# Kernel tuning notes

Measured on AMD Instinct MI355X. Metric: run time of the kernel, lower is better.

Reference implementation:

```python
import jax, jax.numpy as jnp
import numpy as np

B, T, C = 16, 1024, 1024
H = 4          # wshare
K = 31         # kernel_size


def setup_inputs() -> dict:
    key = jax.random.key(0)
    ks = jax.random.split(key, 8)
    s = 1.0 / np.sqrt(C)
    return {
        "query": jax.random.normal(ks[0], (B, T, C), jnp.float32),
        "key_t": jax.random.normal(ks[1], (B, T, C), jnp.float32),   # unused, API compat
        "value": jax.random.normal(ks[2], (B, T, C), jnp.float32),   # unused, API compat
        "mask": jnp.ones((B, 1, T), jnp.int32),
        "W1": jax.random.uniform(ks[3], (2 * C, C), jnp.float32, -s, s),
        "b1": jnp.zeros((2 * C,), jnp.float32),
        "W2": jax.random.uniform(ks[4], (C, C), jnp.float32, -s, s),
        "b2": jnp.zeros((C,), jnp.float32),
        "conv_w": jax.random.uniform(ks[5], (H, K), jnp.float32, 0.0, 1.0),
        "bias": jnp.zeros((C,), jnp.float32),
    }


def reference(query, key_t, value, mask, W1, b1, W2, b2, conv_w, bias):
    # linear1 + GLU: (B,T,C) -> (B,T,2C) -> (B,T,C)
    x = query @ W1.T + b1
    a, g = jnp.split(x, 2, axis=-1)
    x = a * jax.nn.sigmoid(g)
    # (B,T,C) -> (B,C,T) -> (B*C/H, H, T); channel c uses shared kernel c % H
    x = jnp.transpose(x, (0, 2, 1)).reshape(B * C // H, H, T)
    # softmax-normalized shared kernels (H,K); dropout_rate=0 (eval)
    w = jax.nn.softmax(conv_w, axis=-1)
    y = jax.lax.conv_general_dilated(
        x, w[:, None, :], window_strides=(1,), padding=[(K // 2, K // 2)],
        feature_group_count=H, dimension_numbers=("NCH", "OIH", "NCH"))
    x = y.reshape(B, C, T) + bias[None, :, None]
    x = jnp.transpose(x, (0, 2, 1))               # (B,T,C)
    # padding mask: (B,1,T) -> transpose(-1,-2) -> (B,T,1), zero masked frames
    m = jnp.transpose(mask, (0, 2, 1))
    x = jnp.where(m == 0, 0.0, x)
    return x @ W2.T + b2
```

## Files before the change

kernel.cpp:

```cpp
#include <hip/hip_runtime.h>

typedef __attribute__((ext_vector_type(8))) __bf16 bf16x8;
typedef __attribute__((ext_vector_type(4))) __bf16 bf16x4;
typedef __attribute__((ext_vector_type(4))) float  f32x4;
typedef __attribute__((ext_vector_type(4))) float  float4v;

#define DEV static __device__ __forceinline__

DEV void gload_lds16(const void* g, void* l) {
  __builtin_amdgcn_global_load_lds(
      (const __attribute__((address_space(1))) void*)g,
      (__attribute__((address_space(3))) void*)l, 16, 0, 0);
}

__global__ void cvt_bf16_kernel(const float* __restrict__ in,
                                __bf16* __restrict__ out, int n4) {
  int stride = gridDim.x * blockDim.x;
  for (int i = blockIdx.x * blockDim.x + threadIdx.x; i < n4; i += stride) {
    float4v v = ((const float4v*)in)[i];
    bf16x4 o;
#pragma unroll
    for (int j = 0; j < 4; ++j) o[j] = (__bf16)v[j];
    ((bf16x4*)out)[i] = o;
  }
}

__global__ void softmax_w_kernel(const float* __restrict__ cw,
                                 float* __restrict__ out) {
  int h = threadIdx.x;
  if (h < 4) {
    float m = cw[h * 31];
#pragma unroll
    for (int k = 1; k < 31; ++k) m = fmaxf(m, cw[h * 31 + k]);
    float e[31];
    float s = 0.f;
#pragma unroll
    for (int k = 0; k < 31; ++k) {
      e[k] = __expf(cw[h * 31 + k] - m);
      s += e[k];
    }
    float inv = 1.f / s;
#pragma unroll
    for (int k = 0; k < 31; ++k) out[h * 31 + k] = e[k] * inv;
  }
}

template <int STORE_BF16>
__global__ __launch_bounds__(512, 2)
void gemm256_kernel(const __bf16* __restrict__ A, const __bf16* __restrict__ Bw,
                    const float* __restrict__ bias, void* __restrict__ Cout,
                    int M, int N, int K, int ntn) {
  __shared__ __align__(16) __bf16 Al[4 * 8192];
  __shared__ __align__(16) __bf16 Bl[4 * 8192];

  const int tid  = threadIdx.x;
  const int lane = tid & 63;
  const int w    = tid >> 6;
  const int wm = w >> 2, wn = w & 3;

  const int nwg = gridDim.x;
  const int cpx = nwg >> 3;
  const int bid = blockIdx.x;
  const int wgid = (bid & 7) * cpx + (bid >> 3);
  const int m0 = (wgid / ntn) * 256;
  const int n0 = (wgid % ntn) * 256;

  const int NT = K >> 6;

  const int scolE = ((((tid & 7) * 16) ^ (((tid >> 3) & 7) << 4)) >> 1);
  const __bf16* __restrict__ Abase = A + (long)m0 * K;
  const __bf16* __restrict__ Bbase = Bw + (long)n0 * K;

  const int l15 = lane & 15;
  const int xk  = (l15 & 7) << 4;
  const int a0  = l15 * 128 + (((lane >> 4) * 16) ^ xk);
  const int a1  = l15 * 128 + ((((lane >> 4) * 16) + 64) ^ xk);
  const int bq  = (wn & 1) * 8192;
  const int b0  = bq + a0;
  const int b1  = bq + a1;

  f32x4 acc[8][4];
#pragma unroll
  for (int i = 0; i < 8; ++i)
#pragma unroll
    for (int j = 0; j < 4; ++j) {
      acc[i][j][0] = 0.f; acc[i][j][1] = 0.f;
      acc[i][j][2] = 0.f; acc[i][j][3] = 0.f;
    }
  bf16x8 af[8], bf[8];

#define ADST(p, mh) (Al + ((p) * 2 + (mh)) * 8192)
#define BDST(p, nh) (Bl + ((p) * 2 + (nh)) * 8192)
#define AWG(p) ((const char*)Al + ((p) * 2 + wm) * 16384)
#define BWG(p) ((const char*)Bl + ((p) * 2 + (wn >> 1)) * 16384)

#define STAGEG(base, groff, ktc, dst)                                         \
  {                                                                           \
    const __bf16* _s = (base) + (long)((groff) + (tid >> 3)) * K + (ktc) + scolE; \
    gload_lds16(_s, (dst) + tid * 8);                                         \
    gload_lds16(_s + (long)64 * K, (dst) + 4096 + tid * 8);                   \
  }

#define PH_MID()                                     \
  __builtin_amdgcn_s_barrier();                      \
  asm volatile("s_waitcnt lgkmcnt(0)" ::: "memory"); \
  __builtin_amdgcn_s_setprio(1);

#define PH_END(VM)                                                    \
  __builtin_amdgcn_s_setprio(0);                                      \
  if ((VM) == 4) asm volatile("s_waitcnt vmcnt(4)" ::: "memory");     \
  if ((VM) == 0) asm volatile("s_waitcnt vmcnt(0)" ::: "memory");     \
  __builtin_amdgcn_s_barrier();

#define RDA(IB, G)                                                \
  _Pragma("unroll") for (int i2 = 0; i2 < 4; ++i2) {              \
    af[i2 * 2 + 0] = *(const bf16x8*)((G) + ((IB) + i2) * 2048 + a0); \
    af[i2 * 2 + 1] = *(const bf16x8*)((G) + ((IB) + i2) * 2048 + a1); \
  }
#define RDB(JB, G)                                                \
  _Pragma("unroll") for (int j2 = 0; j2 < 2; ++j2) {              \
    bf[(JB) * 2 + j2 * 2 + 0] = *(const bf16x8*)((G) + ((JB) + j2) * 2048 + b0); \
    bf[(JB) * 2 + j2 * 2 + 1] = *(const bf16x8*)((G) + ((JB) + j2) * 2048 + b1); \
  }

#define MMQ(IB, JB)                                                           \
  _Pragma("unroll") for (int i2 = 0; i2 < 4; ++i2)                            \
  _Pragma("unroll") for (int j2 = 0; j2 < 2; ++j2)                            \
  _Pragma("unroll") for (int kk = 0; kk < 2; ++kk)                            \
      acc[(IB) + i2][(JB) + j2] = __builtin_amdgcn_mfma_f32_16x16x32_bf16(    \
          af[i2 * 2 + kk], bf[(JB) * 2 + j2 * 2 + kk], acc[(IB) + i2][(JB) + j2], 0, 0, 0);

  STAGEG(Abase, 0,   0, ADST(0, 0));
  STAGEG(Abase, 128, 0, ADST(0, 1));
  STAGEG(Bbase, 0,   0, BDST(0, 0));
  STAGEG(Bbase, 128, 0, BDST(0, 1));
  asm volatile("s_waitcnt vmcnt(0)" ::: "memory");
  __builtin_amdgcn_s_barrier();

#define TILE(tt, CUR)                                        \
  {                                                          \
    const int ktn = (((tt) + 1 < NT) ? (tt) + 1 : NT - 1) * 64; \
                                                    \
    RDA(0, AWG(CUR)); RDB(0, BWG(CUR));                      \
    STAGEG(Abase, 0,   ktn, ADST(CUR ^ 1, 0));               \
    STAGEG(Abase, 128, ktn, ADST(CUR ^ 1, 1));               \
    PH_MID(); MMQ(0, 0); PH_END(9);                          \
                                                    \
    RDB(2, BWG(CUR));                                        \
    STAGEG(Bbase, 0,   ktn, BDST(CUR ^ 1, 0));               \
    STAGEG(Bbase, 128, ktn, BDST(CUR ^ 1, 1));               \
    PH_MID(); MMQ(0, 2); PH_END(9);                          \
                                                    \
    RDA(4, AWG(CUR));                                        \
    PH_MID(); MMQ(4, 0); PH_END(4);                          \
                                                    \
    PH_MID(); MMQ(4, 2); PH_END(0);                          \
  }

#pragma unroll 1
  for (int t2 = 0; t2 < NT; t2 += 2) {
    TILE(t2, 0);
    TILE(t2 + 1, 1);
  }

  asm volatile("s_waitcnt vmcnt(0)" ::: "memory");

  const int crow = (lane >> 4) * 4;
  const int ccol = lane & 15;
#pragma unroll
  for (int i = 0; i < 8; ++i) {
#pragma unroll
    for (int j = 0; j < 4; ++j) {
      const int mrow = m0 + wm * 128 + i * 16 + crow;
      const int ncol = n0 + wn * 64 + j * 16 + ccol;
      const float bv = bias[ncol];
#pragma unroll
      for (int r = 0; r < 4; ++r) {
        float v = acc[i][j][r] + bv;
        if (STORE_BF16)
          ((__bf16*)Cout)[(long)(mrow + r) * N + ncol] = (__bf16)v;
        else
          ((float*)Cout)[(long)(mrow + r) * N + ncol] = v;
      }
    }
  }
#undef TILE
#undef STAGEG
#undef PH_MID
#undef PH_END
#undef RDA
#undef RDB
#undef MMQ
#undef ADST
#undef BDST
#undef AWG
#undef BWG
}

__global__ __launch_bounds__(256, 2)
void glu_conv_kernel(const __bf16* __restrict__ X, const float* __restrict__ Wsm,
                     const float* __restrict__ bias, const int* __restrict__ mask,
                     __bf16* __restrict__ Y) {
  const int b  = blockIdx.z;
  const int t0 = blockIdx.y * 64;
  const int c0 = blockIdx.x * 128;
  __shared__ float sgT[128][128];
  __shared__ float swl[124];
  const int tid = threadIdx.x;
  if (tid < 124) swl[tid] = Wsm[tid];

  for (int i = tid; i < 2048; i += 256) {
    const int ttl = i & 127;
    const int cg  = i >> 7;
    if (ttl < 94) {
      const int t = t0 - 15 + ttl;
      float v[8];
      if (t >= 0 && t < 1024) {
        const __bf16* p = X + ((long)(b * 1024 + t)) * 2048 + c0 + cg * 8;
        bf16x8 a8 = *(const bf16x8*)p;
        bf16x8 g8 = *(const bf16x8*)(p + 1024);
#pragma unroll
        for (int j = 0; j < 8; ++j) {
          float av = (float)a8[j], gv = (float)g8[j];
          v[j] = av / (1.f + __expf(-gv));
        }
      } else {
#pragma unroll
        for (int j = 0; j < 8; ++j) v[j] = 0.f;
      }
      const int q = ttl >> 2, e = ttl & 3;
#pragma unroll
      for (int j = 0; j < 8; ++j) {
        const int c = cg * 8 + j;
        sgT[c][((q ^ ((c & 7) << 2)) << 2) + e] = v[j];
      }
    }
  }
  __syncthreads();

  const int cc = tid & 127;
  const int th = tid >> 7;
  const int c  = c0 + cc;
  const float* wrow = swl + (c & 3) * 31;
  const float bv = bias[c];
  float acc[32];
#pragma unroll
  for (int u = 0; u < 32; ++u) acc[u] = bv;
  const int key = (cc & 7) << 2;
#pragma unroll
  for (int qi = 0; qi < 16; ++qi) {
    const int q = th * 8 + qi;
    const f32x4 w4 = *(const f32x4*)&sgT[cc][(q ^ key) << 2];
#pragma unroll
    for (int j = 0; j < 4; ++j) {
      const int rl = qi * 4 + j;
#pragma unroll
      for (int u = 0; u < 32; ++u) {
        const int k = rl - u;
        if (k >= 0 && k < 31) acc[u] += w4[j] * wrow[k];
      }
    }
  }
  const long yb = (long)b * 1024 * 1024;
#pragma unroll
  for (int u = 0; u < 32; ++u) {
    const int gt = t0 + th * 32 + u;
    float v = acc[u];
    if (mask[b * 1024 + gt] == 0) v = 0.f;
    Y[yb + (long)gt * 1024 + c] = (__bf16)v;
  }
}

extern "C" void kernel_launch(void* const* d_in, const int* in_sizes, int n_in,
                              void* d_out, int out_size, void* d_ws, size_t ws_size,
                              hipStream_t stream) {
  const float* q    = (const float*)d_in[0];
  const int*   mask = (const int*)d_in[3];
  const float* W1   = (const float*)d_in[4];
  const float* b1   = (const float*)d_in[5];
  const float* W2   = (const float*)d_in[6];
  const float* b2   = (const float*)d_in[7];
  const float* cw   = (const float*)d_in[8];
  const float* bias = (const float*)d_in[9];

  char* ws = (char*)d_ws;
  __bf16* q_bf  = (__bf16*)(ws);
  __bf16* w1_bf = (__bf16*)(ws + (32u << 20));
  __bf16* w2_bf = (__bf16*)(ws + (36u << 20));
  float*  swm   = (float*)(ws + (38u << 20));
  __bf16* x1    = (__bf16*)d_out;
  __bf16* y_bf  = q_bf;

  cvt_bf16_kernel<<<2048, 256, 0, stream>>>(q, q_bf, 16 * 1024 * 1024 / 4);
  cvt_bf16_kernel<<<512, 256, 0, stream>>>(W1, w1_bf, 2048 * 1024 / 4);
  cvt_bf16_kernel<<<256, 256, 0, stream>>>(W2, w2_bf, 1024 * 1024 / 4);
  softmax_w_kernel<<<1, 64, 0, stream>>>(cw, swm);

  gemm256_kernel<1><<<512, 512, 0, stream>>>(q_bf, w1_bf, b1, (void*)x1,
                                             16384, 2048, 1024, 8);
  glu_conv_kernel<<<dim3(8, 16, 16), 256, 0, stream>>>(x1, swm, bias, mask, y_bf);
  gemm256_kernel<0><<<256, 512, 0, stream>>>(y_bf, w2_bf, b2, d_out,
                                             16384, 1024, 1024, 4);
}
```

Baseline: 186.1 us.

## Fuse GLU into first GEMM epilogue via interleaved W1 row permutation

```diff
diff --git a/kernel.cpp b/kernel.cpp
--- a/kernel.cpp
+++ b/kernel.cpp
@@ -25,10 +25,26 @@
   }
 }
 
-__global__ void softmax_w_kernel(const float* __restrict__ cw,
-                                 float* __restrict__ out) {
-  int h = threadIdx.x;
-  if (h < 4) {
+__global__ void cvt_w1_perm_kernel(const float* __restrict__ W1,
+                                   __bf16* __restrict__ out) {
+  const int tid = threadIdx.x;
+  const int r   = blockIdx.x * 2 + (tid >> 7);
+  const int col = (tid & 127) * 8;
+  const int src = (r >> 1) + (r & 1) * 1024;
+  const float* p = W1 + (long)src * 1024 + col;
+  float4v v0 = *(const float4v*)p;
+  float4v v1 = *(const float4v*)(p + 4);
+  bf16x8 o;
+#pragma unroll
+  for (int j = 0; j < 4; ++j) { o[j] = (__bf16)v0[j]; o[4 + j] = (__bf16)v1[j]; }
+  *(bf16x8*)(out + (long)r * 1024 + col) = o;
+}
+
+__global__ void prep_kernel(const float* __restrict__ cw, const float* __restrict__ b1,
+                            float* __restrict__ swm, float* __restrict__ b1p) {
+  const int tid = threadIdx.x;
+  if (tid < 4) {
+    const int h = tid;
     float m = cw[h * 31];
 #pragma unroll
     for (int k = 1; k < 31; ++k) m = fmaxf(m, cw[h * 31 + k]);
@@ -41,15 +57,16 @@
     }
     float inv = 1.f / s;
 #pragma unroll
-    for (int k = 0; k < 31; ++k) out[h * 31 + k] = e[k] * inv;
-  }
-}
-
-template <int STORE_BF16>
-__global__ __launch_bounds__(512, 2)
-void gemm256_kernel(const __bf16* __restrict__ A, const __bf16* __restrict__ Bw,
-                    const float* __restrict__ bias, void* __restrict__ Cout,
-                    int M, int N, int K, int ntn) {
+    for (int k = 0; k < 31; ++k) swm[h * 31 + k] = e[k] * inv;
+  }
+  for (int i = tid; i < 2048; i += 256)
+    b1p[i] = b1[(i >> 1) + (i & 1) * 1024];
+}
+
+template <int MODE>
+DEV void gemm_body(const __bf16* __restrict__ A, const __bf16* __restrict__ Bw,
+                   const float* __restrict__ bias, void* __restrict__ Cout,
+                   int M, int N, int K, int ntn) {
   __shared__ __align__(16) __bf16 Al[4 * 8192];
   __shared__ __align__(16) __bf16 Bl[4 * 8192];
 
@@ -77,7 +94,7 @@
   const int a1  = l15 * 128 + ((((lane >> 4) * 16) + 64) ^ xk);
   const int bq  = (wn & 1) * 8192;
   const int b0  = bq + a0;
-  const int b1  = bq + a1;
+  const int b1r = bq + a1;
 
   f32x4 acc[8][4];
 #pragma unroll
@@ -94,11 +111,11 @@
 #define AWG(p) ((const char*)Al + ((p) * 2 + wm) * 16384)
 #define BWG(p) ((const char*)Bl + ((p) * 2 + (wn >> 1)) * 16384)
 
-#define STAGEG(base, groff, ktc, dst)                                         \
-  {                                                                           \
+#define STAGEG(base, groff, ktc, dst)                                             \
+  {                                                                               \
     const __bf16* _s = (base) + (long)((groff) + (tid >> 3)) * K + (ktc) + scolE; \
-    gload_lds16(_s, (dst) + tid * 8);                                         \
-    gload_lds16(_s + (long)64 * K, (dst) + 4096 + tid * 8);                   \
+    gload_lds16(_s, (dst) + tid * 8);                                             \
+    gload_lds16(_s + (long)64 * K, (dst) + 4096 + tid * 8);                       \
   }
 
 #define PH_MID()                                     \
@@ -112,15 +129,15 @@
   if ((VM) == 0) asm volatile("s_waitcnt vmcnt(0)" ::: "memory");     \
   __builtin_amdgcn_s_barrier();
 
-#define RDA(IB, G)                                                \
-  _Pragma("unroll") for (int i2 = 0; i2 < 4; ++i2) {              \
+#define RDA(IB, G)                                                    \
+  _Pragma("unroll") for (int i2 = 0; i2 < 4; ++i2) {                  \
     af[i2 * 2 + 0] = *(const bf16x8*)((G) + ((IB) + i2) * 2048 + a0); \
     af[i2 * 2 + 1] = *(const bf16x8*)((G) + ((IB) + i2) * 2048 + a1); \
   }
-#define RDB(JB, G)                                                \
-  _Pragma("unroll") for (int j2 = 0; j2 < 2; ++j2) {              \
-    bf[(JB) * 2 + j2 * 2 + 0] = *(const bf16x8*)((G) + ((JB) + j2) * 2048 + b0); \
-    bf[(JB) * 2 + j2 * 2 + 1] = *(const bf16x8*)((G) + ((JB) + j2) * 2048 + b1); \
+#define RDB(JB, G)                                                                \
+  _Pragma("unroll") for (int j2 = 0; j2 < 2; ++j2) {                              \
+    bf[(JB) * 2 + j2 * 2 + 0] = *(const bf16x8*)((G) + ((JB) + j2) * 2048 + b0);  \
+    bf[(JB) * 2 + j2 * 2 + 1] = *(const bf16x8*)((G) + ((JB) + j2) * 2048 + b1r); \
   }
 
 #define MMQ(IB, JB)                                                           \
@@ -137,24 +154,20 @@
   asm volatile("s_waitcnt vmcnt(0)" ::: "memory");
   __builtin_amdgcn_s_barrier();
 
-#define TILE(tt, CUR)                                        \
-  {                                                          \
+#define TILE(tt, CUR)                                           \
+  {                                                             \
     const int ktn = (((tt) + 1 < NT) ? (tt) + 1 : NT - 1) * 64; \
-                                                    \
-    RDA(0, AWG(CUR)); RDB(0, BWG(CUR));                      \
-    STAGEG(Abase, 0,   ktn, ADST(CUR ^ 1, 0));               \
-    STAGEG(Abase, 128, ktn, ADST(CUR ^ 1, 1));               \
-    PH_MID(); MMQ(0, 0); PH_END(9);                          \
-                                                    \
-    RDB(2, BWG(CUR));                                        \
-    STAGEG(Bbase, 0,   ktn, BDST(CUR ^ 1, 0));               \
-    STAGEG(Bbase, 128, ktn, BDST(CUR ^ 1, 1));               \
-    PH_MID(); MMQ(0, 2); PH_END(9);                          \
-                                                    \
-    RDA(4, AWG(CUR));                                        \
-    PH_MID(); MMQ(4, 0); PH_END(4);                          \
-                                                    \
-    PH_MID(); MMQ(4, 2); PH_END(0);                          \
+    RDA(0, AWG(CUR)); RDB(0, BWG(CUR));                         \
+    STAGEG(Abase, 0,   ktn, ADST(CUR ^ 1, 0));                  \
+    STAGEG(Abase, 128, ktn, ADST(CUR ^ 1, 1));                  \
+    PH_MID(); MMQ(0, 0); PH_END(9);                             \
+    RDB(2, BWG(CUR));                                           \
+    STAGEG(Bbase, 0,   ktn, BDST(CUR ^ 1, 0));                  \
+    STAGEG(Bbase, 128, ktn, BDST(CUR ^ 1, 1));                  \
+    PH_MID(); MMQ(0, 2); PH_END(9);                             \
+    RDA(4, AWG(CUR));                                           \
+    PH_MID(); MMQ(4, 0); PH_END(4);                             \
+    PH_MID(); MMQ(4, 2); PH_END(0);                             \
   }
 
 #pragma unroll 1
@@ -177,10 +190,15 @@
 #pragma unroll
       for (int r = 0; r < 4; ++r) {
         float v = acc[i][j][r] + bv;
-        if (STORE_BF16)
-          ((__bf16*)Cout)[(long)(mrow + r) * N + ncol] = (__bf16)v;
-        else
+        if (MODE == 0) {
           ((float*)Cout)[(long)(mrow + r) * N + ncol] = v;
+        } else {
+          float o = __shfl_xor(v, 1);
+          if (!(lane & 1)) {
+            float res = v / (1.f + __expf(-o));
+            ((__bf16*)Cout)[(long)(mrow + r) * (N >> 1) + (ncol >> 1)] = (__bf16)res;
+          }
+        }
       }
     }
   }
@@ -197,10 +215,24 @@
 #undef BWG
 }
 
+__global__ __launch_bounds__(512, 2)
+void gemm1_glu_kernel(const __bf16* __restrict__ A, const __bf16* __restrict__ Bw,
+                      const float* __restrict__ bias, void* __restrict__ Cout,
+                      int M, int N, int K, int ntn) {
+  gemm_body<1>(A, Bw, bias, Cout, M, N, K, ntn);
+}
+
+__global__ __launch_bounds__(512, 2)
+void gemm2_out_kernel(const __bf16* __restrict__ A, const __bf16* __restrict__ Bw,
+                      const float* __restrict__ bias, void* __restrict__ Cout,
+                      int M, int N, int K, int ntn) {
+  gemm_body<0>(A, Bw, bias, Cout, M, N, K, ntn);
+}
+
 __global__ __launch_bounds__(256, 2)
-void glu_conv_kernel(const __bf16* __restrict__ X, const float* __restrict__ Wsm,
-                     const float* __restrict__ bias, const int* __restrict__ mask,
-                     __bf16* __restrict__ Y) {
+void conv_kernel(const __bf16* __restrict__ Yin, const float* __restrict__ Wsm,
+                 const float* __restrict__ bias, const int* __restrict__ mask,
+                 __bf16* __restrict__ Y) {
   const int b  = blockIdx.z;
   const int t0 = blockIdx.y * 64;
   const int c0 = blockIdx.x * 128;
@@ -216,14 +248,9 @@
       const int t = t0 - 15 + ttl;
       float v[8];
       if (t >= 0 && t < 1024) {
-        const __bf16* p = X + ((long)(b * 1024 + t)) * 2048 + c0 + cg * 8;
-        bf16x8 a8 = *(const bf16x8*)p;
-        bf16x8 g8 = *(const bf16x8*)(p + 1024);
-#pragma unroll
-        for (int j = 0; j < 8; ++j) {
-          float av = (float)a8[j], gv = (float)g8[j];
-          v[j] = av / (1.f + __expf(-gv));
-        }
+        bf16x8 a8 = *(const bf16x8*)(Yin + ((long)(b * 1024 + t)) * 1024 + c0 + cg * 8);
+#pragma unroll
+        for (int j = 0; j < 8; ++j) v[j] = (float)a8[j];
       } else {
 #pragma unroll
         for (int j = 0; j < 8; ++j) v[j] = 0.f;
@@ -285,20 +312,21 @@
 
   char* ws = (char*)d_ws;
   __bf16* q_bf  = (__bf16*)(ws);
-  __bf16* w1_bf = (__bf16*)(ws + (32u << 20));
+  __bf16* w1p   = (__bf16*)(ws + (32u << 20));
   __bf16* w2_bf = (__bf16*)(ws + (36u << 20));
   float*  swm   = (float*)(ws + (38u << 20));
-  __bf16* x1    = (__bf16*)d_out;
-  __bf16* y_bf  = q_bf;
+  float*  b1p   = (float*)(ws + (38u << 20) + 4096);
+  __bf16* y     = (__bf16*)d_out;
+  __bf16* yc    = q_bf;
 
   cvt_bf16_kernel<<<2048, 256, 0, stream>>>(q, q_bf, 16 * 1024 * 1024 / 4);
-  cvt_bf16_kernel<<<512, 256, 0, stream>>>(W1, w1_bf, 2048 * 1024 / 4);
+  cvt_w1_perm_kernel<<<1024, 256, 0, stream>>>(W1, w1p);
   cvt_bf16_kernel<<<256, 256, 0, stream>>>(W2, w2_bf, 1024 * 1024 / 4);
-  softmax_w_kernel<<<1, 64, 0, stream>>>(cw, swm);
-
-  gemm256_kernel<1><<<512, 512, 0, stream>>>(q_bf, w1_bf, b1, (void*)x1,
-                                             16384, 2048, 1024, 8);
-  glu_conv_kernel<<<dim3(8, 16, 16), 256, 0, stream>>>(x1, swm, bias, mask, y_bf);
-  gemm256_kernel<0><<<256, 512, 0, stream>>>(y_bf, w2_bf, b2, d_out,
-                                             16384, 1024, 1024, 4);
-}
+  prep_kernel<<<1, 256, 0, stream>>>(cw, b1, swm, b1p);
+
+  gemm1_glu_kernel<<<512, 512, 0, stream>>>(q_bf, w1p, b1p, (void*)y,
+                                            16384, 2048, 1024, 8);
+  conv_kernel<<<dim3(8, 16, 16), 256, 0, stream>>>(y, swm, bias, mask, yc);
+  gemm2_out_kernel<<<256, 512, 0, stream>>>(yc, w2_bf, b2, d_out,
+                                            16384, 1024, 1024, 4);
+}
```

After: 183.6 us. Within noise of the previous version (-1.3%).
